# Optimization experiments

Measured on AMD Instinct MI355X. Metric: run time of the kernel, lower is better.

The kernel has to match this reference:

```python
import jax, jax.numpy as jnp
import numpy as np

V = 50000      # vocab_size
E = 300        # EMBED_SIZE
H = 128        # HIDDEN_SIZE // NUM_DIRS
T = 12         # num_tags
SOS = 3
EOS = 4
NEG = -10000.0


def setup_inputs() -> dict:
    key = jax.random.key(0)
    ks = jax.random.split(key, 14)
    B, S = 128, 512
    x = jax.random.randint(ks[0], (B, S), 0, V)
    y0 = jax.random.randint(ks[1], (B, S), 0, T)
    s = 1.0 / np.sqrt(H)
    u = lambda k, shape: jax.random.uniform(k, shape, jnp.float32, -s, s)
    embed = jax.random.normal(ks[2], (V, E), jnp.float32)
    # torch LSTM gate layout: [i, f, g, o] stacked along first dim (4H)
    Wih_f = u(ks[3], (4 * H, E)); Whh_f = u(ks[4], (4 * H, H)); b_f = u(ks[5], (4 * H,)) + u(ks[6], (4 * H,))
    Wih_b = u(ks[7], (4 * H, E)); Whh_b = u(ks[8], (4 * H, H)); b_b = u(ks[9], (4 * H,)) + u(ks[10], (4 * H,))
    Wout = u(ks[11], (T, 2 * H)); bout = u(ks[12], (T,))
    trans = jax.random.normal(ks[13], (T, T), jnp.float32)
    trans = trans.at[SOS, :].set(NEG).at[:, EOS].set(NEG)
    return dict(x=x, y0=y0, embed=embed,
                Wih_f=Wih_f, Whh_f=Whh_f, b_f=b_f,
                Wih_b=Wih_b, Whh_b=Whh_b, b_b=b_b,
                Wout=Wout, bout=bout, trans=trans)


def _lstm_dir(emb, Wih, Whh, b):
    # emb: [B, S, E] -> hidden states [B, S, H] for one direction
    B = emb.shape[0]
    def step(carry, x_t):
        h, c = carry
        g = x_t @ Wih.T + h @ Whh.T + b  # [B, 4H]
        i, f, gg, o = jnp.split(g, 4, axis=-1)
        c = jax.nn.sigmoid(f) * c + jax.nn.sigmoid(i) * jnp.tanh(gg)
        h = jax.nn.sigmoid(o) * jnp.tanh(c)
        return (h, c), h
    init = (jnp.zeros((B, H), emb.dtype), jnp.zeros((B, H), emb.dtype))
    _, hs = jax.lax.scan(step, init, jnp.swapaxes(emb, 0, 1))  # hs: [S, B, H]
    return jnp.swapaxes(hs, 0, 1)


def reference(x, y0, embed, Wih_f, Whh_f, b_f, Wih_b, Whh_b, b_b, Wout, bout, trans):
    # ---- lstm: embed -> biLSTM -> linear, emissions y: [B, S, T]
    emb = embed[x]
    hf = _lstm_dir(emb, Wih_f, Whh_f, b_f)
    hb = _lstm_dir(emb[:, ::-1], Wih_b, Whh_b, b_b)[:, ::-1]
    y = jnp.concatenate([hf, hb], axis=-1) @ Wout.T + bout

    B = x.shape[0]
    # ---- CRF partition Z via forward algorithm (trans[i, j] = score j -> i)
    score0 = jnp.full((B, T), NEG, y.dtype).at[:, SOS].set(0.0)
    def step(score, emit_t):
        new = jax.nn.logsumexp(score[:, None, :] + trans[None, :, :], axis=-1) + emit_t
        return new, None
    scoreZ, _ = jax.lax.scan(step, score0, jnp.swapaxes(y, 0, 1))
    Z = jax.nn.logsumexp(scoreZ + trans[EOS][None, :], axis=-1)  # [B]

    # ---- gold path score (vectorized version of crf.score)
    y0p = jnp.concatenate([jnp.full((B, 1), SOS, y0.dtype), y0], axis=1)  # [B, S+1]
    emit = jnp.take_along_axis(y, y0p[:, 1:, None], axis=2)[..., 0].sum(axis=1)
    tr = trans[y0p[:, 1:], y0p[:, :-1]].sum(axis=1)
    gold = emit + tr + trans[EOS, y0p[:, -1]]

    return Z - gold  # [B] negative log-likelihood per example
```

## Files before the change

kernel.cpp:

```cpp
#include <hip/hip_runtime.h>

typedef unsigned short u16;
typedef __attribute__((ext_vector_type(8))) short short8;
typedef __attribute__((ext_vector_type(4))) float floatx4;

#define SOS 3
#define EOS 4
#define NEGV -10000.0f
#define LOG2E 1.442695041f
#define TWOLOG2E 2.885390082f

__device__ __forceinline__ u16 f2bf(float f) {
  union { float f; unsigned int i; } v; v.f = f;
  unsigned int r = (v.i + 0x7FFFu + ((v.i >> 16) & 1u)) >> 16;
  return (u16)r;
}
__device__ __forceinline__ void gload_lds16(const u16* g, u16* l) {
  __builtin_amdgcn_global_load_lds((const __attribute__((address_space(1))) void*)g,
                                   (__attribute__((address_space(3))) void*)l, 16, 0, 0);
}

__global__ __launch_bounds__(256) void gather_kernel(const float* __restrict__ embed,
                                                     const int* __restrict__ x,
                                                     u16* __restrict__ A) {
  int idx = blockIdx.x * 256 + threadIdx.x;
  int row = idx / 40;
  int c8 = idx - row * 40;
  int col0 = c8 * 8;
  int b = row & 127, t = row >> 7;
  const float* src = embed + (size_t)x[b * 512 + t] * 300 + col0;
  short8 o;
  if (col0 + 8 <= 300) {
    float4 f0 = *(const float4*)(src);
    float4 f1 = *(const float4*)(src + 4);
    o[0] = (short)f2bf(f0.x); o[1] = (short)f2bf(f0.y);
    o[2] = (short)f2bf(f0.z); o[3] = (short)f2bf(f0.w);
    o[4] = (short)f2bf(f1.x); o[5] = (short)f2bf(f1.y);
    o[6] = (short)f2bf(f1.z); o[7] = (short)f2bf(f1.w);
  } else {
    #pragma unroll
    for (int e = 0; e < 8; ++e)
      o[e] = (col0 + e < 300) ? (short)f2bf(src[e]) : (short)0;
  }
  *(short8*)&A[(size_t)row * 320 + col0] = o;
}

__global__ __launch_bounds__(256) void wpack_kernel(const float* __restrict__ Wf,
                                                    const float* __restrict__ Wb,
                                                    u16* __restrict__ Wp) {
  int idx = blockIdx.x * 256 + threadIdx.x;
  int p = idx / 40;
  int c8 = idx - p * 40;
  int col0 = c8 * 8;
  int dd = p >> 9, q = p & 511;
  int j = q >> 2, g = q & 3;
  const float* src = (dd ? Wb : Wf) + (size_t)(g * 128 + j) * 300;
  short8 o;
  #pragma unroll
  for (int e = 0; e < 8; ++e)
    o[e] = (col0 + e < 300) ? (short)f2bf(src[col0 + e]) : (short)0;
  *(short8*)&Wp[(size_t)p * 320 + col0] = o;
}

__global__ __launch_bounds__(256) void gemm_kernel(const u16* __restrict__ A,
                                                   const u16* __restrict__ B,
                                                   const float* __restrict__ bf_,
                                                   const float* __restrict__ bb_,
                                                   u16* __restrict__ G) {
  __shared__ u16 At[128 * 32];
  __shared__ u16 Bt[128 * 32];
  const int n = blockIdx.x;
  const int xcd = n & 7, rr = n >> 3;
  const int bx = xcd * 64 + (rr >> 3);
  const int by = rr & 7;
  const int tid = threadIdx.x;
  const int lane = tid & 63;
  const int wave = tid >> 6;
  const int wr = wave >> 1, wc = wave & 1;
  const int arow0 = bx * 128;
  const int bcol0 = by * 128;
  floatx4 acc[4][4] = {};
  const int fq = lane >> 4;
  const int fr = lane & 15;
  const int sr = wave * 32 + (lane >> 2);
  const int sc = (lane & 3) * 8;
  for (int k0 = 0; k0 < 320; k0 += 32) {
    #pragma unroll
    for (int q = 0; q < 2; ++q) {
      gload_lds16(&A[(size_t)(arow0 + sr + q * 16) * 320 + k0 + sc], &At[wave * 1024 + q * 512]);
      gload_lds16(&B[(size_t)(bcol0 + sr + q * 16) * 320 + k0 + sc], &Bt[wave * 1024 + q * 512]);
    }
    __syncthreads();
    short8 af[4], bfr[4];
    #pragma unroll
    for (int mi = 0; mi < 4; ++mi)
      af[mi] = *(const short8*)&At[(wr * 64 + mi * 16 + fr) * 32 + fq * 8];
    #pragma unroll
    for (int ni = 0; ni < 4; ++ni)
      bfr[ni] = *(const short8*)&Bt[(wc * 64 + ni * 16 + fr) * 32 + fq * 8];
    #pragma unroll
    for (int mi = 0; mi < 4; ++mi)
      #pragma unroll
      for (int ni = 0; ni < 4; ++ni)
        acc[mi][ni] = __builtin_amdgcn_mfma_f32_16x16x32_bf16(af[mi], bfr[ni], acc[mi][ni], 0, 0, 0);
    __syncthreads();
  }
  float biasv[4];
  #pragma unroll
  for (int ni = 0; ni < 4; ++ni) {
    int col = bcol0 + wc * 64 + ni * 16 + fr;
    int dd = col >> 9, q = col & 511;
    int jj = q >> 2, gg = q & 3;
    biasv[ni] = (dd ? bb_ : bf_)[gg * 128 + jj];
  }
  #pragma unroll
  for (int mi = 0; mi < 4; ++mi)
    #pragma unroll
    for (int ni = 0; ni < 4; ++ni)
      #pragma unroll
      for (int r = 0; r < 4; ++r) {
        int row = arow0 + wr * 64 + mi * 16 + fq * 4 + r;
        int col = bcol0 + wc * 64 + ni * 16 + fr;
        G[(size_t)row * 1024 + col] = f2bf(acc[mi][ni][r] + biasv[ni]);
      }
}

__global__ __launch_bounds__(512, 2) void lstm_fused_kernel(const u16* __restrict__ Gp,
                                                            const float* __restrict__ Whh_f,
                                                            const float* __restrict__ Whh_b,
                                                            u16* __restrict__ hs) {
  const int bid = blockIdx.x;
  const int d  = bid >> 5;
  const int b0 = (bid & 31) * 4;
  const int tid = threadIdx.x;
  const int w = tid >> 6, lane = tid & 63;
  const int fr = lane & 15, fq = lane >> 4;
  const float* Wd = d ? Whh_b : Whh_f;

  short8 Wfr[4][4];
  #pragma unroll
  for (int tt = 0; tt < 4; ++tt) {
    const int orow = (fr & 3) * 128 + (16 * w + 4 * tt + (fr >> 2));
    #pragma unroll
    for (int kk = 0; kk < 4; ++kk) {
      const float* src = Wd + (size_t)orow * 128 + fq * 8 + kk * 32;
      float4 x0 = *(const float4*)src;
      float4 x1 = *(const float4*)(src + 4);
      short8 o;
      o[0] = (short)f2bf(x0.x); o[1] = (short)f2bf(x0.y);
      o[2] = (short)f2bf(x0.z); o[3] = (short)f2bf(x0.w);
      o[4] = (short)f2bf(x1.x); o[5] = (short)f2bf(x1.y);
      o[6] = (short)f2bf(x1.z); o[7] = (short)f2bf(x1.w);
      Wfr[tt][kk] = o;
    }
  }

  __shared__ __align__(16) u16 hbuf[2][512];
  for (int i = tid; i < 1024; i += 512) (&hbuf[0][0])[i] = 0;
  __syncthreads();

  const int ts = d ? -1 : 1;
  const int t0 = d ? 511 : 0;
  const int bb  = fr & 3;
  const int ttl = fr >> 2;
  const int jj  = 16 * w + 4 * ttl + fq;

  const int ho0 = bb * 128 + (((fq      + 4 * bb) & 15) << 3);
  const int ho1 = bb * 128 + (((fq + 4  + 4 * bb) & 15) << 3);
  const int ho2 = bb * 128 + (((fq + 8  + 4 * bb) & 15) << 3);
  const int ho3 = bb * 128 + (((fq + 12 + 4 * bb) & 15) << 3);
  const int hwi = bb * 128 + ((((jj >> 3) + 4 * bb) & 15) << 3) + (jj & 7);

  const long long gstep = (long long)ts * 131072;
  const long long hstep = (long long)ts * 256;
  const u16* gld = Gp + (long long)t0 * 131072 + (b0 + bb) * 1024 + d * 512 + 4 * jj;
  u16* hsp = hs + (size_t)(b0 + bb) * 131072 + (long long)t0 * 256 + d * 128 + jj;
  float cst = 0.f;

  uint2 gA, gB, gC;
  gA = *(const uint2*)gld; gld += gstep;
  gB = *(const uint2*)gld; gld += gstep;
  gC = *(const uint2*)gld; gld += gstep;

  u16* hr = &hbuf[0][0];
  u16* hw = &hbuf[1][0];

#define STEPN(GR_, PF_) { \
    short8 f0 = *(const short8*)(hr + ho0); \
    short8 f1 = *(const short8*)(hr + ho1); \
    short8 f2 = *(const short8*)(hr + ho2); \
    short8 f3 = *(const short8*)(hr + ho3); \
    floatx4 a0 = {0.f, 0.f, 0.f, 0.f}; \
    floatx4 a1 = a0, a2 = a0, a3 = a0; \
    a0 = __builtin_amdgcn_mfma_f32_16x16x32_bf16(Wfr[0][0], f0, a0, 0, 0, 0); \
    a1 = __builtin_amdgcn_mfma_f32_16x16x32_bf16(Wfr[1][0], f0, a1, 0, 0, 0); \
    a2 = __builtin_amdgcn_mfma_f32_16x16x32_bf16(Wfr[2][0], f0, a2, 0, 0, 0); \
    a3 = __builtin_amdgcn_mfma_f32_16x16x32_bf16(Wfr[3][0], f0, a3, 0, 0, 0); \
    a0 = __builtin_amdgcn_mfma_f32_16x16x32_bf16(Wfr[0][1], f1, a0, 0, 0, 0); \
    a1 = __builtin_amdgcn_mfma_f32_16x16x32_bf16(Wfr[1][1], f1, a1, 0, 0, 0); \
    a2 = __builtin_amdgcn_mfma_f32_16x16x32_bf16(Wfr[2][1], f1, a2, 0, 0, 0); \
    a3 = __builtin_amdgcn_mfma_f32_16x16x32_bf16(Wfr[3][1], f1, a3, 0, 0, 0); \
    a0 = __builtin_amdgcn_mfma_f32_16x16x32_bf16(Wfr[0][2], f2, a0, 0, 0, 0); \
    a1 = __builtin_amdgcn_mfma_f32_16x16x32_bf16(Wfr[1][2], f2, a1, 0, 0, 0); \
    a2 = __builtin_amdgcn_mfma_f32_16x16x32_bf16(Wfr[2][2], f2, a2, 0, 0, 0); \
    a3 = __builtin_amdgcn_mfma_f32_16x16x32_bf16(Wfr[3][2], f2, a3, 0, 0, 0); \
    a0 = __builtin_amdgcn_mfma_f32_16x16x32_bf16(Wfr[0][3], f3, a0, 0, 0, 0); \
    a1 = __builtin_amdgcn_mfma_f32_16x16x32_bf16(Wfr[1][3], f3, a1, 0, 0, 0); \
    a2 = __builtin_amdgcn_mfma_f32_16x16x32_bf16(Wfr[2][3], f3, a2, 0, 0, 0); \
    a3 = __builtin_amdgcn_mfma_f32_16x16x32_bf16(Wfr[3][3], f3, a3, 0, 0, 0); \
    const bool s0 = (ttl & 1), s1 = (ttl & 2); \
    float p0 = s1 ? (s0 ? a3[0] : a2[0]) : (s0 ? a1[0] : a0[0]); \
    float p1 = s1 ? (s0 ? a3[1] : a2[1]) : (s0 ? a1[1] : a0[1]); \
    float p2 = s1 ? (s0 ? a3[2] : a2[2]) : (s0 ? a1[2] : a0[2]); \
    float p3 = s1 ? (s0 ? a3[3] : a2[3]) : (s0 ? a1[3] : a0[3]); \
    float G0 = __builtin_bit_cast(float, GR_.x << 16); \
    float G1 = __builtin_bit_cast(float, GR_.x & 0xffff0000u); \
    float G2 = __builtin_bit_cast(float, GR_.y << 16); \
    float G3 = __builtin_bit_cast(float, GR_.y & 0xffff0000u); \
    if (PF_) { GR_ = *(const uint2*)gld; gld += gstep; } \
    float i_ = p0 + G0, f_ = p1 + G1, g_ = p2 + G2, o_ = p3 + G3; \
    float p  = __builtin_amdgcn_exp2f(__builtin_amdgcn_fmed3f(g_ * TWOLOG2E, -40.f, 40.f)); \
    float qi = __builtin_amdgcn_exp2f(__builtin_amdgcn_fmed3f(i_ * -LOG2E, -40.f, 40.f)); \
    float qf = __builtin_amdgcn_exp2f(__builtin_amdgcn_fmed3f(f_ * -LOG2E, -40.f, 40.f)); \
    float qo = __builtin_amdgcn_exp2f(__builtin_amdgcn_fmed3f(o_ * -LOG2E, -40.f, 40.f)); \
    float D1 = (1.f + qi) * (p + 1.f); \
    float qf1 = 1.f + qf; \
    float cn = (cst * D1 + (p - 1.f) * qf1) * __builtin_amdgcn_rcpf(qf1 * D1); \
    cst = cn; \
    float v = __builtin_amdgcn_exp2f(__builtin_amdgcn_fmed3f(cn * TWOLOG2E, -40.f, 40.f)); \
    float h = (v - 1.f) * __builtin_amdgcn_rcpf((1.f + qo) * (v + 1.f)); \
    u16 hb = f2bf(h); \
    hw[hwi] = hb; \
    *hsp = hb; \
    hsp += hstep; \
    __builtin_amdgcn_sched_barrier(0); \
    asm volatile("s_waitcnt lgkmcnt(0)"); \
    __builtin_amdgcn_sched_barrier(0); \
    __builtin_amdgcn_s_barrier(); \
    __builtin_amdgcn_sched_barrier(0); \
    u16* tp_ = hr; hr = hw; hw = tp_; \
  }

  #pragma unroll 1
  for (int it = 0; it < 170; ++it) {
    STEPN(gA, true);
    STEPN(gB, true);
    STEPN(gC, true);
  }
  STEPN(gA, false);
  STEPN(gB, false);
#undef STEPN
}

__global__ __launch_bounds__(256) void emis_kernel(const u16* __restrict__ hs,
                                                   const float* __restrict__ Wout,
                                                   const float* __restrict__ bout,
                                                   float* __restrict__ y) {
  __shared__ float Ws[12 * 256];
  __shared__ float bs[12];
  const int tid = threadIdx.x;
  for (int i = tid; i < 12 * 256; i += 256) Ws[i] = Wout[i];
  if (tid < 12) bs[tid] = bout[tid];
  __syncthreads();
  const int wave = tid >> 6, lane = tid & 63;
  const size_t m = (size_t)blockIdx.x * 4 + wave;
  uint2 hv = *(const uint2*)&hs[m * 256 + lane * 4];
  float h0 = __builtin_bit_cast(float, hv.x << 16);
  float h1 = __builtin_bit_cast(float, hv.x & 0xffff0000u);
  float h2 = __builtin_bit_cast(float, hv.y << 16);
  float h3 = __builtin_bit_cast(float, hv.y & 0xffff0000u);
  float p[12];
  #pragma unroll
  for (int tg = 0; tg < 12; ++tg) {
    const float* wv = &Ws[tg * 256 + lane * 4];
    p[tg] = h0 * wv[0] + h1 * wv[1] + h2 * wv[2] + h3 * wv[3];
  }
  #pragma unroll
  for (int off = 32; off; off >>= 1)
    #pragma unroll
    for (int tg = 0; tg < 12; ++tg)
      p[tg] += __shfl_xor(p[tg], off);
  if (lane == 0) {
    #pragma unroll
    for (int tg = 0; tg < 12; ++tg)
      y[m * 12 + tg] = p[tg] + bs[tg];
  }
}

__global__ __launch_bounds__(64) void crf_kernel(const float* __restrict__ y,
                                                 const int* __restrict__ y0,
                                                 const float* __restrict__ trans,
                                                 float* __restrict__ out) {
  const int b = blockIdx.x;
  const int lane = threadIdx.x;
  __shared__ float trs[144];
  for (int i = lane; i < 144; i += 64) trs[i] = trans[i];
  __syncthreads();
  float etr[12];
  #pragma unroll
  for (int jj = 0; jj < 12; ++jj) etr[jj] = 0.f;
  float z = NEGV, treos = 0.f;
  if (lane < 12) {
    #pragma unroll
    for (int jj = 0; jj < 12; ++jj) etr[jj] = __expf(trs[lane * 12 + jj]);
    z = (lane == SOS) ? 0.f : NEGV;
    treos = trs[EOS * 12 + lane];
  }
  float base = 0.f;
  const float* yb = y + (size_t)b * 512 * 12;
  float e0 = (lane < 12) ? yb[lane] : 0.f;
  float e1 = (lane < 12) ? yb[12 + lane] : 0.f;
  for (int t = 0; t < 512; ++t) {
    float emit = e0;
    e0 = e1;
    if (t + 2 < 512 && lane < 12) e1 = yb[(t + 2) * 12 + lane];
    float zj[12];
    #pragma unroll
    for (int jj = 0; jj < 12; ++jj) zj[jj] = __shfl(z, jj);
    float l = 0.f;
    if (lane < 12) {
      float ex[12];
      #pragma unroll
      for (int jj = 0; jj < 12; ++jj) ex[jj] = __expf(zj[jj]) * etr[jj];
      float sum = (((ex[0] + ex[1]) + (ex[2] + ex[3])) + ((ex[4] + ex[5]) + (ex[6] + ex[7])))
                + ((ex[8] + ex[9]) + (ex[10] + ex[11]));
      l = __logf(sum) + emit;
    }
    float l0 = __shfl(l, 0);
    z = l - l0;
    base += l0;
  }
  float v = (lane < 12) ? z + treos : -INFINITY;
  float M2 = v;
  #pragma unroll
  for (int off = 32; off; off >>= 1) M2 = fmaxf(M2, __shfl_xor(M2, off));
  float e = __expf(v - M2);
  #pragma unroll
  for (int off = 32; off; off >>= 1) e += __shfl_xor(e, off);
  const float Z = base + M2 + __logf(e);
  const int* y0b = y0 + (size_t)b * 512;
  float acc = 0.f;
  for (int t = lane; t < 512; t += 64) {
    int cur = y0b[t];
    int prev = t ? y0b[t - 1] : SOS;
    acc += yb[t * 12 + cur] + trs[cur * 12 + prev];
  }
  #pragma unroll
  for (int off = 32; off; off >>= 1) acc += __shfl_xor(acc, off);
  if (lane == 0) {
    float gold = acc + trs[EOS * 12 + y0b[511]];
    out[b] = Z - gold;
  }
}

extern "C" void kernel_launch(void* const* d_in, const int* in_sizes, int n_in,
                              void* d_out, int out_size, void* d_ws, size_t ws_size,
                              hipStream_t stream) {
  (void)in_sizes; (void)n_in; (void)out_size; (void)ws_size;
  const int*   x     = (const int*)d_in[0];
  const int*   y0    = (const int*)d_in[1];
  const float* embed = (const float*)d_in[2];
  const float* Wih_f = (const float*)d_in[3];
  const float* Whh_f = (const float*)d_in[4];
  const float* b_f   = (const float*)d_in[5];
  const float* Wih_b = (const float*)d_in[6];
  const float* Whh_b = (const float*)d_in[7];
  const float* b_b   = (const float*)d_in[8];
  const float* Wout  = (const float*)d_in[9];
  const float* bout  = (const float*)d_in[10];
  const float* trans = (const float*)d_in[11];
  float* out = (float*)d_out;

  char* ws = (char*)d_ws;
  u16*   A  = (u16*)(ws);
  u16*   Wp = (u16*)(ws + 41943040);
  u16*   G  = (u16*)(ws + 42598400);
  u16*   hs = (u16*)(ws + 176816128);
  float* yy = (float*)(ws + 210370560);

  gather_kernel<<<10240, 256, 0, stream>>>(embed, x, A);
  wpack_kernel<<<160, 256, 0, stream>>>(Wih_f, Wih_b, Wp);
  gemm_kernel<<<4096, 256, 0, stream>>>(A, Wp, b_f, b_b, G);
  lstm_fused_kernel<<<64, 512, 0, stream>>>(G, Whh_f, Whh_b, hs);
  emis_kernel<<<16384, 256, 0, stream>>>(hs, Wout, bout, yy);
  crf_kernel<<<128, 64, 0, stream>>>(yy, y0, trans, out);
}
```

Measured before the change: 552.1 us.

## Merge gather and weight-pack kernels, batch emission rows, streamline CRF recurrence

New measurement: 581.6 us. 5.3% more time.

```diff
diff --git a/kernel.cpp b/kernel.cpp
--- a/kernel.cpp
+++ b/kernel.cpp
@@ -20,46 +20,47 @@
                                    (__attribute__((address_space(3))) void*)l, 16, 0, 0);
 }
 
-__global__ __launch_bounds__(256) void gather_kernel(const float* __restrict__ embed,
-                                                     const int* __restrict__ x,
-                                                     u16* __restrict__ A) {
-  int idx = blockIdx.x * 256 + threadIdx.x;
-  int row = idx / 40;
-  int c8 = idx - row * 40;
-  int col0 = c8 * 8;
-  int b = row & 127, t = row >> 7;
-  const float* src = embed + (size_t)x[b * 512 + t] * 300 + col0;
-  short8 o;
-  if (col0 + 8 <= 300) {
-    float4 f0 = *(const float4*)(src);
-    float4 f1 = *(const float4*)(src + 4);
-    o[0] = (short)f2bf(f0.x); o[1] = (short)f2bf(f0.y);
-    o[2] = (short)f2bf(f0.z); o[3] = (short)f2bf(f0.w);
-    o[4] = (short)f2bf(f1.x); o[5] = (short)f2bf(f1.y);
-    o[6] = (short)f2bf(f1.z); o[7] = (short)f2bf(f1.w);
+__global__ __launch_bounds__(256) void gw_kernel(const float* __restrict__ embed,
+                                                 const int* __restrict__ x,
+                                                 const float* __restrict__ Wf,
+                                                 const float* __restrict__ Wb,
+                                                 u16* __restrict__ A,
+                                                 u16* __restrict__ Wp) {
+  if (blockIdx.x < 10240) {
+    int idx = blockIdx.x * 256 + threadIdx.x;
+    int row = idx / 40;
+    int c8 = idx - row * 40;
+    int col0 = c8 * 8;
+    int b = row & 127, t = row >> 7;
+    const float* src = embed + (size_t)x[b * 512 + t] * 300 + col0;
+    short8 o;
+    if (col0 + 8 <= 300) {
+      float4 f0 = *(const float4*)(src);
+      float4 f1 = *(const float4*)(src + 4);
+      o[0] = (short)f2bf(f0.x); o[1] = (short)f2bf(f0.y);
+      o[2] = (short)f2bf(f0.z); o[3] = (short)f2bf(f0.w);
+      o[4] = (short)f2bf(f1.x); o[5] = (short)f2bf(f1.y);
+      o[6] = (short)f2bf(f1.z); o[7] = (short)f2bf(f1.w);
+    } else {
+      #pragma unroll
+      for (int e = 0; e < 8; ++e)
+        o[e] = (col0 + e < 300) ? (short)f2bf(src[e]) : (short)0;
+    }
+    *(short8*)&A[(size_t)row * 320 + col0] = o;
   } else {
+    int idx = (blockIdx.x - 10240) * 256 + threadIdx.x;
+    int p = idx / 40;
+    int c8 = idx - p * 40;
+    int col0 = c8 * 8;
+    int dd = p >> 9, q = p & 511;
+    int j = q >> 2, g = q & 3;
+    const float* src = (dd ? Wb : Wf) + (size_t)(g * 128 + j) * 300;
+    short8 o;
     #pragma unroll
     for (int e = 0; e < 8; ++e)
-      o[e] = (col0 + e < 300) ? (short)f2bf(src[e]) : (short)0;
-  }
-  *(short8*)&A[(size_t)row * 320 + col0] = o;
-}
-
-__global__ __launch_bounds__(256) void wpack_kernel(const float* __restrict__ Wf,
-                                                    const float* __restrict__ Wb,
-                                                    u16* __restrict__ Wp) {
-  int idx = blockIdx.x * 256 + threadIdx.x;
-  int p = idx / 40;
-  int c8 = idx - p * 40;
-  int col0 = c8 * 8;
-  int dd = p >> 9, q = p & 511;
-  int j = q >> 2, g = q & 3;
-  const float* src = (dd ? Wb : Wf) + (size_t)(g * 128 + j) * 300;
-  short8 o;
-  #pragma unroll
-  for (int e = 0; e < 8; ++e)
-    o[e] = (col0 + e < 300) ? (short)f2bf(src[col0 + e]) : (short)0;
-  *(short8*)&Wp[(size_t)p * 320 + col0] = o;
+      o[e] = (col0 + e < 300) ? (short)f2bf(src[col0 + e]) : (short)0;
+    *(short8*)&Wp[(size_t)p * 320 + col0] = o;
+  }
 }
 
 __global__ __launch_bounds__(256) void gemm_kernel(const u16* __restrict__ A,
@@ -263,27 +264,30 @@
   if (tid < 12) bs[tid] = bout[tid];
   __syncthreads();
   const int wave = tid >> 6, lane = tid & 63;
-  const size_t m = (size_t)blockIdx.x * 4 + wave;
-  uint2 hv = *(const uint2*)&hs[m * 256 + lane * 4];
-  float h0 = __builtin_bit_cast(float, hv.x << 16);
-  float h1 = __builtin_bit_cast(float, hv.x & 0xffff0000u);
-  float h2 = __builtin_bit_cast(float, hv.y << 16);
-  float h3 = __builtin_bit_cast(float, hv.y & 0xffff0000u);
-  float p[12];
-  #pragma unroll
-  for (int tg = 0; tg < 12; ++tg) {
-    const float* wv = &Ws[tg * 256 + lane * 4];
-    p[tg] = h0 * wv[0] + h1 * wv[1] + h2 * wv[2] + h3 * wv[3];
-  }
-  #pragma unroll
-  for (int off = 32; off; off >>= 1)
-    #pragma unroll
-    for (int tg = 0; tg < 12; ++tg)
-      p[tg] += __shfl_xor(p[tg], off);
-  if (lane == 0) {
-    #pragma unroll
-    for (int tg = 0; tg < 12; ++tg)
-      y[m * 12 + tg] = p[tg] + bs[tg];
+  #pragma unroll
+  for (int it = 0; it < 4; ++it) {
+    const size_t m = ((size_t)blockIdx.x * 4 + it) * 4 + wave;
+    uint2 hv = *(const uint2*)&hs[m * 256 + lane * 4];
+    float h0 = __builtin_bit_cast(float, hv.x << 16);
+    float h1 = __builtin_bit_cast(float, hv.x & 0xffff0000u);
+    float h2 = __builtin_bit_cast(float, hv.y << 16);
+    float h3 = __builtin_bit_cast(float, hv.y & 0xffff0000u);
+    float p[12];
+    #pragma unroll
+    for (int tg = 0; tg < 12; ++tg) {
+      const float* wv = &Ws[tg * 256 + lane * 4];
+      p[tg] = h0 * wv[0] + h1 * wv[1] + h2 * wv[2] + h3 * wv[3];
+    }
+    #pragma unroll
+    for (int off = 32; off; off >>= 1)
+      #pragma unroll
+      for (int tg = 0; tg < 12; ++tg)
+        p[tg] += __shfl_xor(p[tg], off);
+    if (lane == 0) {
+      #pragma unroll
+      for (int tg = 0; tg < 12; ++tg)
+        y[m * 12 + tg] = p[tg] + bs[tg];
+    }
   }
 }
 
@@ -296,37 +300,40 @@
   __shared__ float trs[144];
   for (int i = lane; i < 144; i += 64) trs[i] = trans[i];
   __syncthreads();
-  float etr[12];
-  #pragma unroll
-  for (int jj = 0; jj < 12; ++jj) etr[jj] = 0.f;
-  float z = NEGV, treos = 0.f;
-  if (lane < 12) {
-    #pragma unroll
-    for (int jj = 0; jj < 12; ++jj) etr[jj] = __expf(trs[lane * 12 + jj]);
-    z = (lane == SOS) ? 0.f : NEGV;
-    treos = trs[EOS * 12 + lane];
-  }
+  float etr[12], etr0[12];
+  float treos = 0.f;
+  const int row = (lane < 12) ? lane : 0;
+  #pragma unroll
+  for (int j = 0; j < 12; ++j) etr[j] = __expf(trs[row * 12 + j]);
+  #pragma unroll
+  for (int j = 0; j < 12; ++j) etr0[j] = __expf(trs[j]);
+  if (lane < 12) treos = trs[EOS * 12 + lane];
+  float z = (lane == SOS) ? 0.f : NEGV;
   float base = 0.f;
   const float* yb = y + (size_t)b * 512 * 12;
-  float e0 = (lane < 12) ? yb[lane] : 0.f;
-  float e1 = (lane < 12) ? yb[12 + lane] : 0.f;
+  const int lr = lane & 15;
+  float e0 = yb[(lr < 12) ? lr : 0];
+  float e1 = yb[12 + ((lr < 12) ? lr : 0)];
   for (int t = 0; t < 512; ++t) {
     float emit = e0;
     e0 = e1;
-    if (t + 2 < 512 && lane < 12) e1 = yb[(t + 2) * 12 + lane];
-    float zj[12];
-    #pragma unroll
-    for (int jj = 0; jj < 12; ++jj) zj[jj] = __shfl(z, jj);
-    float l = 0.f;
-    if (lane < 12) {
-      float ex[12];
-      #pragma unroll
-      for (int jj = 0; jj < 12; ++jj) ex[jj] = __expf(zj[jj]) * etr[jj];
-      float sum = (((ex[0] + ex[1]) + (ex[2] + ex[3])) + ((ex[4] + ex[5]) + (ex[6] + ex[7])))
-                + ((ex[8] + ex[9]) + (ex[10] + ex[11]));
-      l = __logf(sum) + emit;
-    }
-    float l0 = __shfl(l, 0);
+    if (t + 2 < 512) e1 = yb[(t + 2) * 12 + ((lr < 12) ? lr : 0)];
+    float emit0 = __builtin_bit_cast(float, __builtin_amdgcn_readlane(__builtin_bit_cast(int, emit), 0));
+    float E[12];
+    #pragma unroll
+    for (int j = 0; j < 12; ++j) {
+      int zj = __builtin_amdgcn_readlane(__builtin_bit_cast(int, z), j);
+      E[j] = __expf(__builtin_bit_cast(float, zj));
+    }
+    float ex[12], ex0[12];
+    #pragma unroll
+    for (int j = 0; j < 12; ++j) { ex[j] = E[j] * etr[j]; ex0[j] = E[j] * etr0[j]; }
+    float s  = (((ex[0] + ex[1]) + (ex[2] + ex[3])) + ((ex[4] + ex[5]) + (ex[6] + ex[7])))
+             + ((ex[8] + ex[9]) + (ex[10] + ex[11]));
+    float s0 = (((ex0[0] + ex0[1]) + (ex0[2] + ex0[3])) + ((ex0[4] + ex0[5]) + (ex0[6] + ex0[7])))
+             + ((ex0[8] + ex0[9]) + (ex0[10] + ex0[11]));
+    float l  = __logf(s)  + emit;
+    float l0 = __logf(s0) + emit0;
     z = l - l0;
     base += l0;
   }
@@ -378,10 +385,9 @@
   u16*   hs = (u16*)(ws + 176816128);
   float* yy = (float*)(ws + 210370560);
 
-  gather_kernel<<<10240, 256, 0, stream>>>(embed, x, A);
-  wpack_kernel<<<160, 256, 0, stream>>>(Wih_f, Wih_b, Wp);
+  gw_kernel<<<10400, 256, 0, stream>>>(embed, x, Wih_f, Wih_b, A, Wp);
   gemm_kernel<<<4096, 256, 0, stream>>>(A, Wp, b_f, b_b, G);
   lstm_fused_kernel<<<64, 512, 0, stream>>>(G, Whh_f, Whh_b, hs);
-  emis_kernel<<<16384, 256, 0, stream>>>(hs, Wout, bout, yy);
+  emis_kernel<<<4096, 256, 0, stream>>>(hs, Wout, bout, yy);
   crf_kernel<<<128, 64, 0, stream>>>(yy, y0, trans, out);
 }
```
